# Kernel tuning notes

Hardware: AMD Instinct MI355X
Metric: run time of the kernel (lower is better)

The kernel has to match this reference:

```python
import jax, jax.numpy as jnp
import numpy as np

DIM = 512
BATCH = 64
SRC_L = 2048


def setup_inputs() -> dict:
    key = jax.random.key(0)
    ks = jax.random.split(key, 7)
    s = 1.0 / np.sqrt(DIM)
    return {
        "query": jax.random.normal(ks[0], (BATCH, DIM), dtype=jnp.float32),
        "ref": jax.random.normal(ks[1], (SRC_L, BATCH, DIM), dtype=jnp.float32),
        # nn.Linear(dim, dim)
        "Wq": jax.random.uniform(ks[2], (DIM, DIM), jnp.float32, -s, s),
        "bq": jax.random.uniform(ks[3], (DIM,), jnp.float32, -s, s),
        # nn.Conv1d(dim, dim, 1, 1) -> weight [out, in, 1] squeezed to [out, in]
        "Wr": jax.random.uniform(ks[4], (DIM, DIM), jnp.float32, -s, s),
        "br": jax.random.uniform(ks[5], (DIM,), jnp.float32, -s, s),
        # self.v ~ U(-1/sqrt(dim), 1/sqrt(dim))
        "v": jax.random.uniform(ks[6], (DIM,), jnpp := jnp.float32, -s, s),
    }


def reference(query, ref, Wq, bq, Wr, br, v):
    # ref: [L, B, D] -> [B, D, L]
    ref_bdl = jnp.transpose(ref, (1, 2, 0))
    # q = Linear(query): [B, D] -> broadcast as [B, D, 1]
    q = query @ Wq.T + bq  # [B, D]
    # e = 1x1 Conv1d over ref: pointwise GEMM along channel dim
    e = jnp.einsum("oi,bil->bol", Wr, ref_bdl) + br[None, :, None]  # [B, D, L]
    # u = v . tanh(q + e) reduced over D (fused broadcast-add-tanh-reduce)
    u = jnp.einsum("d,bdl->bl", v, jnp.tanh(q[:, :, None] + e))  # [B, L]
    logits = u  # use_tanh=False
    return (e, logits)
```

## Files before the change

kernel.cpp:

```cpp
#include <hip/hip_runtime.h>

#define DIM 512
#define B_  64
#define L_  2048

typedef unsigned short u16;
typedef float f32x4 __attribute__((ext_vector_type(4)));
typedef short s16x8 __attribute__((ext_vector_type(8)));
typedef short s16x4 __attribute__((ext_vector_type(4)));

__device__ __forceinline__ u16 f2bf(float f) {
  union { float f; unsigned u; } x{f};
  unsigned r = x.u + 0x7FFFu + ((x.u >> 16) & 1u);
  return (u16)(r >> 16);
}

__device__ __forceinline__ float tanh_fast(float x) {
  float e2 = __expf(2.0f * x);
  return 1.0f - 2.0f / (e2 + 1.0f);
}

__global__ __launch_bounds__(256) void prep_kernel(
    const float* __restrict__ query, const float* __restrict__ Wq,
    const float* __restrict__ bq, const float* __restrict__ Wr,
    float* __restrict__ q_out, u16* __restrict__ Wrbt) {
  const int blk = blockIdx.x;
  const int tid = threadIdx.x;
  if (blk < 64) {
    __shared__ float qs[DIM];
    for (int i = tid; i < DIM; i += 256) qs[i] = query[blk * DIM + i];
    __syncthreads();
    for (int o = tid; o < DIM; o += 256) {
      const float* w = Wq + o * DIM;
      float acc = 0.f;
      for (int k = 0; k < DIM; k += 4) {
        f32x4 a = *(const f32x4*)&qs[k];
        f32x4 b = *(const f32x4*)&w[k];
        acc += a.x * b.x + a.y * b.y + a.z * b.z + a.w * b.w;
      }
      q_out[blk * DIM + o] = acc + bq[o];
    }
  } else {
    const int c = blk - 64;
    const int flat = c * 4096 + tid * 16;
    const int o = flat >> 9, k0 = flat & 511;
    const int t = k0 >> 5, kk = k0 & 31;
    u16* dst = Wrbt + t * 16384 + o * 32 + kk;
#pragma unroll
    for (int i = 0; i < 4; ++i) {
      f32x4 a = *(const f32x4*)&Wr[flat + i * 4];
      s16x4 o4;
      o4.x = (short)f2bf(a.x); o4.y = (short)f2bf(a.y);
      o4.z = (short)f2bf(a.z); o4.w = (short)f2bf(a.w);
      *(s16x4*)&dst[i * 4] = o4;
    }
  }
}

__global__ __launch_bounds__(1024, 4) void gemm_fused(
    const float* __restrict__ ref, const u16* __restrict__ Wrbt,
    const float* __restrict__ q, const float* __restrict__ br,
    const float* __restrict__ v, float* __restrict__ e_out,
    float* __restrict__ logits) {
  __shared__ u16 Bs[2][128 * 40];
  __shared__ float Ebuf[2][32 * 132];
  __shared__ float u_lds[16][64];

  const int b = blockIdx.x, lt = blockIdx.y;
  const int l0 = lt * 128;
  const int tid = threadIdx.x, lane = tid & 63, wid = tid >> 6;
  const int og = wid >> 1, lg = wid & 1;
  const int rr = lane & 15, kg = lane >> 4;
  const int srow = tid >> 3, sc8 = tid & 7;

  const size_t refbase = ((size_t)(l0 + srow) * 64 + b) * 512 + sc8 * 4;
  const u16* ap = Wrbt + (og * 64 + rr) * 32 + kg * 8;

  f32x4 srIF;
  s16x8 afP[4], afQ[4];
  {
    f32x4 a = __builtin_nontemporal_load((const f32x4*)&ref[refbase]);
    s16x4 o4;
    o4.x = (short)f2bf(a.x); o4.y = (short)f2bf(a.y);
    o4.z = (short)f2bf(a.z); o4.w = (short)f2bf(a.w);
    *(s16x4*)&Bs[0][srow * 40 + sc8 * 4] = o4;
    srIF = __builtin_nontemporal_load((const f32x4*)&ref[refbase + 32]);
#pragma unroll
    for (int fm = 0; fm < 4; ++fm)
      afP[fm] = *(const s16x8*)(ap + fm * 512);
  }
  asm volatile("s_waitcnt lgkmcnt(0)" ::: "memory");
  __builtin_amdgcn_s_barrier();
  __builtin_amdgcn_sched_barrier(0);

  f32x4 acc[4][4];
#pragma unroll
  for (int fm = 0; fm < 4; ++fm)
#pragma unroll
    for (int fn = 0; fn < 4; ++fn) acc[fm][fn] = (f32x4){0.f, 0.f, 0.f, 0.f};

#pragma unroll
  for (int tt = 0; tt < 8; ++tt) {
    const int t0 = tt * 2, t1 = t0 + 1;
    {
      f32x4 srN;
      if (t0 < 14)
        srN = __builtin_nontemporal_load((const f32x4*)&ref[refbase + (t0 + 2) * 32]);
#pragma unroll
      for (int fm = 0; fm < 4; ++fm)
        afQ[fm] = *(const s16x8*)(ap + t1 * 16384 + fm * 512);
      s16x8 bf[4];
#pragma unroll
      for (int fn = 0; fn < 4; ++fn)
        bf[fn] = *(const s16x8*)&Bs[0][(lg * 64 + fn * 16 + rr) * 40 + kg * 8];
      __builtin_amdgcn_s_setprio(1);
#pragma unroll
      for (int fm = 0; fm < 4; ++fm)
#pragma unroll
        for (int fn = 0; fn < 4; ++fn)
          acc[fm][fn] = __builtin_amdgcn_mfma_f32_16x16x32_bf16(bf[fn], afP[fm], acc[fm][fn], 0, 0, 0);
      __builtin_amdgcn_s_setprio(0);
      {
        s16x4 o4;
        o4.x = (short)f2bf(srIF.x); o4.y = (short)f2bf(srIF.y);
        o4.z = (short)f2bf(srIF.z); o4.w = (short)f2bf(srIF.w);
        *(s16x4*)&Bs[1][srow * 40 + sc8 * 4] = o4;
      }
      asm volatile("s_waitcnt lgkmcnt(0)" ::: "memory");
      __builtin_amdgcn_s_barrier();
      __builtin_amdgcn_sched_barrier(0);
      if (t0 < 14) srIF = srN;
    }
    {
      f32x4 srN;
      if (t1 < 14)
        srN = __builtin_nontemporal_load((const f32x4*)&ref[refbase + (t1 + 2) * 32]);
      if (t1 < 15)
#pragma unroll
        for (int fm = 0; fm < 4; ++fm)
          afP[fm] = *(const s16x8*)(ap + (t1 + 1) * 16384 + fm * 512);
      s16x8 bf[4];
#pragma unroll
      for (int fn = 0; fn < 4; ++fn)
        bf[fn] = *(const s16x8*)&Bs[1][(lg * 64 + fn * 16 + rr) * 40 + kg * 8];
      __builtin_amdgcn_s_setprio(1);
#pragma unroll
      for (int fm = 0; fm < 4; ++fm)
#pragma unroll
        for (int fn = 0; fn < 4; ++fn)
          acc[fm][fn] = __builtin_amdgcn_mfma_f32_16x16x32_bf16(bf[fn], afQ[fm], acc[fm][fn], 0, 0, 0);
      __builtin_amdgcn_s_setprio(0);
      if (t1 < 15) {
        {
          s16x4 o4;
          o4.x = (short)f2bf(srIF.x); o4.y = (short)f2bf(srIF.y);
          o4.z = (short)f2bf(srIF.z); o4.w = (short)f2bf(srIF.w);
          *(s16x4*)&Bs[0][srow * 40 + sc8 * 4] = o4;
        }
        asm volatile("s_waitcnt lgkmcnt(0)" ::: "memory");
        __builtin_amdgcn_s_barrier();
        __builtin_amdgcn_sched_barrier(0);
        if (t1 < 14) srIF = srN;
      }
    }
  }

  float bb[4];
  f32x4 usA[4];
#pragma unroll
  for (int fn = 0; fn < 4; ++fn) usA[fn] = (f32x4){0.f, 0.f, 0.f, 0.f};
#pragma unroll
  for (int fm = 0; fm < 4; ++fm) {
    const int o = og * 64 + fm * 16 + rr;
    bb[fm] = br[o];
    const float qv = q[b * DIM + o] + bb[fm];
    const float vv = v[o];
#pragma unroll
    for (int fn = 0; fn < 4; ++fn) {
      f32x4 a = acc[fm][fn];
      f32x4 th;
      th.x = tanh_fast(a.x + qv);
      th.y = tanh_fast(a.y + qv);
      th.z = tanh_fast(a.z + qv);
      th.w = tanh_fast(a.w + qv);
      usA[fn] += vv * th;
    }
  }
#pragma unroll
  for (int fn = 0; fn < 4; ++fn) {
    f32x4 us = usA[fn];
#pragma unroll
    for (int msk = 1; msk <= 8; msk <<= 1) {
      us.x += __shfl_xor(us.x, msk);
      us.y += __shfl_xor(us.y, msk);
      us.z += __shfl_xor(us.z, msk);
      us.w += __shfl_xor(us.w, msk);
    }
    if (rr == 0)
      *(f32x4*)&u_lds[wid][fn * 16 + kg * 4] = us;
  }

#pragma unroll 2
  for (int ph = 0; ph < 16; ++ph) {
    float* Eb = &Ebuf[ph & 1][0];
    if (og == (ph >> 1)) {
      const int f2b = (ph & 1) * 2;
#pragma unroll
      for (int f2 = 0; f2 < 2; ++f2) {
        const int fm = f2b + f2;
#pragma unroll
        for (int fn = 0; fn < 4; ++fn) {
          f32x4 ev = acc[fm][fn] + bb[fm];
          *(f32x4*)&Eb[(f2 * 16 + rr) * 132 + lg * 64 + fn * 16 + kg * 4] = ev;
        }
      }
    }
    __syncthreads();
    {
      const int op = tid >> 5, lc4 = (tid & 31) * 4;
      f32x4 ev = *(const f32x4*)&Eb[op * 132 + lc4];
      __builtin_nontemporal_store(
          ev, (f32x4*)&e_out[((size_t)(b * DIM + ph * 32 + op)) * L_ + l0 + lc4]);
    }
  }

  __syncthreads();
  if (tid < 128) {
    const int ll = tid & 63, lgi = tid >> 6;
    float s = 0.f;
#pragma unroll
    for (int o8 = 0; o8 < 8; ++o8) s += u_lds[o8 * 2 + lgi][ll];
    logits[(size_t)b * L_ + l0 + lgi * 64 + ll] = s;
  }
}

extern "C" void kernel_launch(void* const* d_in, const int* in_sizes, int n_in,
                              void* d_out, int out_size, void* d_ws, size_t ws_size,
                              hipStream_t stream) {
  const float* query = (const float*)d_in[0];
  const float* ref   = (const float*)d_in[1];
  const float* Wq    = (const float*)d_in[2];
  const float* bq    = (const float*)d_in[3];
  const float* Wr    = (const float*)d_in[4];
  const float* br    = (const float*)d_in[5];
  const float* v     = (const float*)d_in[6];

  float* e_out  = (float*)d_out;
  float* logits = e_out + (size_t)B_ * DIM * L_;

  char* ws = (char*)d_ws;
  u16*   Wrbt = (u16*)ws;
  float* q    = (float*)(ws + 524288);

  prep_kernel<<<128, 256, 0, stream>>>(query, Wq, bq, Wr, q, Wrbt);
  gemm_fused<<<dim3(64, 16), 1024, 0, stream>>>(ref, Wrbt, q, br, v, e_out, logits);
}
```

Baseline: 214.9 us.

## Make fused GEMM kernel persistent with two tiles per block

Launches 512 blocks that each loop over two (batch, L-tile) work items instead of 1024 one-shot blocks, reusing the same LDS buffers. The aim is to cut block launch and tail overhead and give each block a single full wave of work on the device. The E-store loop now uses an extra waitcnt+barrier after each phase instead of a single syncthreads, which is needed for buffer reuse across iterations but adds synchronisation. There is no overlap between one tile's epilogue and the next tile's loads, so each block's two tiles run strictly one after the other.

```diff
diff --git a/kernel.cpp b/kernel.cpp
--- a/kernel.cpp
+++ b/kernel.cpp
@@ -8,6 +8,13 @@
 typedef float f32x4 __attribute__((ext_vector_type(4)));
 typedef short s16x8 __attribute__((ext_vector_type(8)));
 typedef short s16x4 __attribute__((ext_vector_type(4)));
+
+#define LGKM_BAR()                                          \
+  do {                                                      \
+    asm volatile("s_waitcnt lgkmcnt(0)" ::: "memory");      \
+    __builtin_amdgcn_s_barrier();                           \
+    __builtin_amdgcn_sched_barrier(0);                      \
+  } while (0)
 
 __device__ __forceinline__ u16 f2bf(float f) {
   union { float f; unsigned u; } x{f};
@@ -66,171 +73,171 @@
   __shared__ float Ebuf[2][32 * 132];
   __shared__ float u_lds[16][64];
 
-  const int b = blockIdx.x, lt = blockIdx.y;
-  const int l0 = lt * 128;
+  const int bid = blockIdx.x;
   const int tid = threadIdx.x, lane = tid & 63, wid = tid >> 6;
   const int og = wid >> 1, lg = wid & 1;
   const int rr = lane & 15, kg = lane >> 4;
   const int srow = tid >> 3, sc8 = tid & 7;
 
-  const size_t refbase = ((size_t)(l0 + srow) * 64 + b) * 512 + sc8 * 4;
   const u16* ap = Wrbt + (og * 64 + rr) * 32 + kg * 8;
 
-  f32x4 srIF;
-  s16x8 afP[4], afQ[4];
-  {
-    f32x4 a = __builtin_nontemporal_load((const f32x4*)&ref[refbase]);
-    s16x4 o4;
-    o4.x = (short)f2bf(a.x); o4.y = (short)f2bf(a.y);
-    o4.z = (short)f2bf(a.z); o4.w = (short)f2bf(a.w);
-    *(s16x4*)&Bs[0][srow * 40 + sc8 * 4] = o4;
-    srIF = __builtin_nontemporal_load((const f32x4*)&ref[refbase + 32]);
+  for (int tp = 0; tp < 2; ++tp) {
+    const int f = bid + tp * 512;
+    const int b = f & 63, lt = f >> 6;
+    const int l0 = lt * 128;
+    const size_t refbase = ((size_t)(l0 + srow) * 64 + b) * 512 + sc8 * 4;
+
+    f32x4 srIF;
+    s16x8 afP[4], afQ[4];
+    {
+      f32x4 a = __builtin_nontemporal_load((const f32x4*)&ref[refbase]);
+      s16x4 o4;
+      o4.x = (short)f2bf(a.x); o4.y = (short)f2bf(a.y);
+      o4.z = (short)f2bf(a.z); o4.w = (short)f2bf(a.w);
+      *(s16x4*)&Bs[0][srow * 40 + sc8 * 4] = o4;
+      srIF = __builtin_nontemporal_load((const f32x4*)&ref[refbase + 32]);
+#pragma unroll
+      for (int fm = 0; fm < 4; ++fm)
+        afP[fm] = *(const s16x8*)(ap + fm * 512);
+    }
+    LGKM_BAR();
+
+    f32x4 acc[4][4];
 #pragma unroll
     for (int fm = 0; fm < 4; ++fm)
-      afP[fm] = *(const s16x8*)(ap + fm * 512);
-  }
-  asm volatile("s_waitcnt lgkmcnt(0)" ::: "memory");
-  __builtin_amdgcn_s_barrier();
-  __builtin_amdgcn_sched_barrier(0);
-
-  f32x4 acc[4][4];
-#pragma unroll
-  for (int fm = 0; fm < 4; ++fm)
-#pragma unroll
-    for (int fn = 0; fn < 4; ++fn) acc[fm][fn] = (f32x4){0.f, 0.f, 0.f, 0.f};
-
-#pragma unroll
-  for (int tt = 0; tt < 8; ++tt) {
-    const int t0 = tt * 2, t1 = t0 + 1;
-    {
-      f32x4 srN;
-      if (t0 < 14)
-        srN = __builtin_nontemporal_load((const f32x4*)&ref[refbase + (t0 + 2) * 32]);
-#pragma unroll
-      for (int fm = 0; fm < 4; ++fm)
-        afQ[fm] = *(const s16x8*)(ap + t1 * 16384 + fm * 512);
-      s16x8 bf[4];
-#pragma unroll
-      for (int fn = 0; fn < 4; ++fn)
-        bf[fn] = *(const s16x8*)&Bs[0][(lg * 64 + fn * 16 + rr) * 40 + kg * 8];
-      __builtin_amdgcn_s_setprio(1);
-#pragma unroll
-      for (int fm = 0; fm < 4; ++fm)
+#pragma unroll
+      for (int fn = 0; fn < 4; ++fn) acc[fm][fn] = (f32x4){0.f, 0.f, 0.f, 0.f};
+
+#pragma unroll
+    for (int tt = 0; tt < 8; ++tt) {
+      const int t0 = tt * 2, t1 = t0 + 1;
+      {
+        f32x4 srN;
+        if (t0 < 14)
+          srN = __builtin_nontemporal_load((const f32x4*)&ref[refbase + (t0 + 2) * 32]);
+#pragma unroll
+        for (int fm = 0; fm < 4; ++fm)
+          afQ[fm] = *(const s16x8*)(ap + t1 * 16384 + fm * 512);
+        s16x8 bf[4];
 #pragma unroll
         for (int fn = 0; fn < 4; ++fn)
-          acc[fm][fn] = __builtin_amdgcn_mfma_f32_16x16x32_bf16(bf[fn], afP[fm], acc[fm][fn], 0, 0, 0);
-      __builtin_amdgcn_s_setprio(0);
-      {
-        s16x4 o4;
-        o4.x = (short)f2bf(srIF.x); o4.y = (short)f2bf(srIF.y);
-        o4.z = (short)f2bf(srIF.z); o4.w = (short)f2bf(srIF.w);
-        *(s16x4*)&Bs[1][srow * 40 + sc8 * 4] = o4;
-      }
-      asm volatile("s_waitcnt lgkmcnt(0)" ::: "memory");
-      __builtin_amdgcn_s_barrier();
-      __builtin_amdgcn_sched_barrier(0);
-      if (t0 < 14) srIF = srN;
-    }
-    {
-      f32x4 srN;
-      if (t1 < 14)
-        srN = __builtin_nontemporal_load((const f32x4*)&ref[refbase + (t1 + 2) * 32]);
-      if (t1 < 15)
+          bf[fn] = *(const s16x8*)&Bs[0][(lg * 64 + fn * 16 + rr) * 40 + kg * 8];
+        __builtin_amdgcn_s_setprio(1);
 #pragma unroll
         for (int fm = 0; fm < 4; ++fm)
-          afP[fm] = *(const s16x8*)(ap + (t1 + 1) * 16384 + fm * 512);
-      s16x8 bf[4];
-#pragma unroll
-      for (int fn = 0; fn < 4; ++fn)
-        bf[fn] = *(const s16x8*)&Bs[1][(lg * 64 + fn * 16 + rr) * 40 + kg * 8];
-      __builtin_amdgcn_s_setprio(1);
-#pragma unroll
-      for (int fm = 0; fm < 4; ++fm)
-#pragma unroll
-        for (int fn = 0; fn < 4; ++fn)
-          acc[fm][fn] = __builtin_amdgcn_mfma_f32_16x16x32_bf16(bf[fn], afQ[fm], acc[fm][fn], 0, 0, 0);
-      __builtin_amdgcn_s_setprio(0);
-      if (t1 < 15) {
+#pragma unroll
+          for (int fn = 0; fn < 4; ++fn)
+            acc[fm][fn] = __builtin_amdgcn_mfma_f32_16x16x32_bf16(bf[fn], afP[fm], acc[fm][fn], 0, 0, 0);
+        __builtin_amdgcn_s_setprio(0);
         {
           s16x4 o4;
           o4.x = (short)f2bf(srIF.x); o4.y = (short)f2bf(srIF.y);
           o4.z = (short)f2bf(srIF.z); o4.w = (short)f2bf(srIF.w);
-          *(s16x4*)&Bs[0][srow * 40 + sc8 * 4] = o4;
+          *(s16x4*)&Bs[1][srow * 40 + sc8 * 4] = o4;
         }
-        asm volatile("s_waitcnt lgkmcnt(0)" ::: "memory");
-        __builtin_amdgcn_s_barrier();
-        __builtin_amdgcn_sched_barrier(0);
-        if (t1 < 14) srIF = srN;
-      }
-    }
-  }
-
-  float bb[4];
-  f32x4 usA[4];
-#pragma unroll
-  for (int fn = 0; fn < 4; ++fn) usA[fn] = (f32x4){0.f, 0.f, 0.f, 0.f};
-#pragma unroll
-  for (int fm = 0; fm < 4; ++fm) {
-    const int o = og * 64 + fm * 16 + rr;
-    bb[fm] = br[o];
-    const float qv = q[b * DIM + o] + bb[fm];
-    const float vv = v[o];
+        LGKM_BAR();
+        if (t0 < 14) srIF = srN;
+      }
+      {
+        f32x4 srN;
+        if (t1 < 14)
+          srN = __builtin_nontemporal_load((const f32x4*)&ref[refbase + (t1 + 2) * 32]);
+        if (t1 < 15)
+#pragma unroll
+          for (int fm = 0; fm < 4; ++fm)
+            afP[fm] = *(const s16x8*)(ap + (t1 + 1) * 16384 + fm * 512);
+        s16x8 bf[4];
+#pragma unroll
+        for (int fn = 0; fn < 4; ++fn)
+          bf[fn] = *(const s16x8*)&Bs[1][(lg * 64 + fn * 16 + rr) * 40 + kg * 8];
+        __builtin_amdgcn_s_setprio(1);
+#pragma unroll
+        for (int fm = 0; fm < 4; ++fm)
+#pragma unroll
+          for (int fn = 0; fn < 4; ++fn)
+            acc[fm][fn] = __builtin_amdgcn_mfma_f32_16x16x32_bf16(bf[fn], afQ[fm], acc[fm][fn], 0, 0, 0);
+        __builtin_amdgcn_s_setprio(0);
+        if (t1 < 15) {
+          {
+            s16x4 o4;
+            o4.x = (short)f2bf(srIF.x); o4.y = (short)f2bf(srIF.y);
+            o4.z = (short)f2bf(srIF.z); o4.w = (short)f2bf(srIF.w);
+            *(s16x4*)&Bs[0][srow * 40 + sc8 * 4] = o4;
+          }
+          LGKM_BAR();
+          if (t1 < 14) srIF = srN;
+        }
+      }
+    }
+
+    float bb[4];
+    f32x4 usA[4];
+#pragma unroll
+    for (int fn = 0; fn < 4; ++fn) usA[fn] = (f32x4){0.f, 0.f, 0.f, 0.f};
+#pragma unroll
+    for (int fm = 0; fm < 4; ++fm) {
+      const int o = og * 64 + fm * 16 + rr;
+      bb[fm] = br[o];
+      const float qv = q[b * DIM + o] + bb[fm];
+      const float vv = v[o];
+#pragma unroll
+      for (int fn = 0; fn < 4; ++fn) {
+        f32x4 a = acc[fm][fn];
+        f32x4 th;
+        th.x = tanh_fast(a.x + qv);
+        th.y = tanh_fast(a.y + qv);
+        th.z = tanh_fast(a.z + qv);
+        th.w = tanh_fast(a.w + qv);
+        usA[fn] += vv * th;
+      }
+    }
 #pragma unroll
     for (int fn = 0; fn < 4; ++fn) {
-      f32x4 a = acc[fm][fn];
-      f32x4 th;
-      th.x = tanh_fast(a.x + qv);
-      th.y = tanh_fast(a.y + qv);
-      th.z = tanh_fast(a.z + qv);
-      th.w = tanh_fast(a.w + qv);
-      usA[fn] += vv * th;
-    }
-  }
-#pragma unroll
-  for (int fn = 0; fn < 4; ++fn) {
-    f32x4 us = usA[fn];
-#pragma unroll
-    for (int msk = 1; msk <= 8; msk <<= 1) {
-      us.x += __shfl_xor(us.x, msk);
-      us.y += __shfl_xor(us.y, msk);
-      us.z += __shfl_xor(us.z, msk);
-      us.w += __shfl_xor(us.w, msk);
-    }
-    if (rr == 0)
-      *(f32x4*)&u_lds[wid][fn * 16 + kg * 4] = us;
-  }
+      f32x4 us = usA[fn];
+#pragma unroll
+      for (int msk = 1; msk <= 8; msk <<= 1) {
+        us.x += __shfl_xor(us.x, msk);
+        us.y += __shfl_xor(us.y, msk);
+        us.z += __shfl_xor(us.z, msk);
+        us.w += __shfl_xor(us.w, msk);
+      }
+      if (rr == 0)
+        *(f32x4*)&u_lds[wid][fn * 16 + kg * 4] = us;
+    }
 
 #pragma unroll 2
-  for (int ph = 0; ph < 16; ++ph) {
-    float* Eb = &Ebuf[ph & 1][0];
-    if (og == (ph >> 1)) {
-      const int f2b = (ph & 1) * 2;
-#pragma unroll
-      for (int f2 = 0; f2 < 2; ++f2) {
-        const int fm = f2b + f2;
-#pragma unroll
-        for (int fn = 0; fn < 4; ++fn) {
-          f32x4 ev = acc[fm][fn] + bb[fm];
-          *(f32x4*)&Eb[(f2 * 16 + rr) * 132 + lg * 64 + fn * 16 + kg * 4] = ev;
+    for (int ph = 0; ph < 16; ++ph) {
+      float* Eb = &Ebuf[ph & 1][0];
+      if (og == (ph >> 1)) {
+        const int f2b = (ph & 1) * 2;
+#pragma unroll
+        for (int f2 = 0; f2 < 2; ++f2) {
+          const int fm = f2b + f2;
+#pragma unroll
+          for (int fn = 0; fn < 4; ++fn) {
+            f32x4 ev = acc[fm][fn] + bb[fm];
+            *(f32x4*)&Eb[(f2 * 16 + rr) * 132 + lg * 64 + fn * 16 + kg * 4] = ev;
+          }
         }
       }
-    }
-    __syncthreads();
-    {
-      const int op = tid >> 5, lc4 = (tid & 31) * 4;
-      f32x4 ev = *(const f32x4*)&Eb[op * 132 + lc4];
-      __builtin_nontemporal_store(
-          ev, (f32x4*)&e_out[((size_t)(b * DIM + ph * 32 + op)) * L_ + l0 + lc4]);
-    }
-  }
-
-  __syncthreads();
-  if (tid < 128) {
-    const int ll = tid & 63, lgi = tid >> 6;
-    float s = 0.f;
-#pragma unroll
-    for (int o8 = 0; o8 < 8; ++o8) s += u_lds[o8 * 2 + lgi][ll];
-    logits[(size_t)b * L_ + l0 + lgi * 64 + ll] = s;
+      LGKM_BAR();
+      {
+        const int op = tid >> 5, lc4 = (tid & 31) * 4;
+        f32x4 ev = *(const f32x4*)&Eb[op * 132 + lc4];
+        __builtin_nontemporal_store(
+            ev, (f32x4*)&e_out[((size_t)(b * DIM + ph * 32 + op)) * L_ + l0 + lc4]);
+      }
+      LGKM_BAR();
+    }
+
+    if (tid < 128) {
+      const int ll = tid & 63, lgi = tid >> 6;
+      float s = 0.f;
+#pragma unroll
+      for (int o8 = 0; o8 < 8; ++o8) s += u_lds[o8 * 2 + lgi][ll];
+      logits[(size_t)b * L_ + l0 + lgi * 64 + ll] = s;
+    }
+    LGKM_BAR();
   }
 }
 
@@ -253,5 +260,5 @@
   float* q    = (float*)(ws + 524288);
 
   prep_kernel<<<128, 256, 0, stream>>>(query, Wq, bq, Wr, q, Wrbt);
-  gemm_fused<<<dim3(64, 16), 1024, 0, stream>>>(ref, Wrbt, q, br, v, e_out, logits);
-}
+  gemm_fused<<<512, 1024, 0, stream>>>(ref, Wrbt, q, br, v, e_out, logits);
+}
```

Result: slower. 398.2 us (+85.3%).
